# Kernel optimization log

Hardware: AMD Instinct MI355X
Metric: run time of the kernel (lower is better)

Reference implementation:

```python
import jax, jax.numpy as jnp
import numpy as np

N = 100000      # nodes
E = 1600000     # edges
D = 128         # embedding_size (num_heads=1)
L = 4           # num_layers
NEG_SLOPE_ATT = 0.2    # GATConv attention LeakyReLU
NEG_SLOPE_ACT = 0.01   # nn.LeakyReLU default
LN_EPS = 1e-5


def leaky(x, s):
    return jnp.where(x > 0, x, s * x)


def layer_norm(x, gamma, beta):
    mu = jnp.mean(x, axis=-1, keepdims=True)
    var = jnp.mean(jnp.square(x - mu), axis=-1, keepdims=True)
    return (x - mu) * jax.lax.rsqrt(var + LN_EPS) * gamma + beta


def gat_conv(x, src, dst, W, a_src, a_dst, b):
    # PyG GATConv, heads=1, add_self_loops=False, no edge features
    h = x @ W                                  # [N, D]
    alpha_src = h @ a_src                      # [N]
    alpha_dst = h @ a_dst                      # [N]
    e = leaky(alpha_src[src] + alpha_dst[dst], NEG_SLOPE_ATT)   # [E]
    # softmax over incoming edges of each destination node
    m = jax.ops.segment_max(e, dst, num_segments=N)             # [N]
    ex = jnp.exp(e - m[dst])
    denom = jax.ops.segment_sum(ex, dst, num_segments=N)        # [N]
    alpha = ex / (denom[dst] + 1e-16)                           # [E]
    out = jax.ops.segment_sum(alpha[:, None] * h[src], dst, num_segments=N)
    return out + b


def setup_inputs() -> dict:
    key = jax.random.key(0)
    ks = jax.random.split(key, 12)
    x = jax.random.normal(ks[0], (N, D), dtype=jnp.float32)
    edge_index = jax.random.randint(ks[1], (2, E), 0, N, dtype=jnp.int32)
    s = 0.05
    return {
        "x": x,
        "edge_index": edge_index,
        "W_in": jax.random.normal(ks[2], (D, D), dtype=jnp.float32) * s,
        "b_in": jnp.zeros((D,), dtype=jnp.float32),
        "Wl": jax.random.normal(ks[3], (L, D, D), dtype=jnp.float32) * s,
        "att_src": jax.random.normal(ks[4], (L, D), dtype=jnp.float32) * s,
        "att_dst": jax.random.normal(ks[5], (L, D), dtype=jnp.float32) * s,
        "bias_l": jnp.zeros((L, D), dtype=jnp.float32),
        "gamma": jnp.ones((L, D), dtype=jnp.float32),
        "beta": jnp.zeros((L, D), dtype=jnp.float32),
    }


def reference(x, edge_index, W_in, b_in, Wl, att_src, att_dst, bias_l, gamma, beta):
    src, dst = edge_index[0], edge_index[1]
    h = leaky(x @ W_in + b_in, NEG_SLOPE_ACT)
    for i in range(L):
        h = gat_conv(h, src, dst, Wl[i], att_src[i], att_dst[i], bias_l[i])
        h = layer_norm(h, gamma[i], beta[i])
        h = leaky(h, NEG_SLOPE_ACT)
        # dropout p=0.3 is identity in eval mode; pooling undefined in source -> identity
    return h
```

## Files before the change

### kernel.cpp

```cpp
#include <hip/hip_runtime.h>
#include <hip/hip_fp16.h>
#include <math.h>

#define NN 100000
#define EE 1600000
#define DD 128
#define NBUCK 196
#define NBLKP 196
#define EPB 8192

typedef _Float16 f16;
typedef f16 f16x8 __attribute__((ext_vector_type(8)));
typedef float f32x4 __attribute__((ext_vector_type(4)));

#define LDA 136
#define WCHUNKS 2304

__global__ __launch_bounds__(256) void part_hist_k(const int* __restrict__ dst, int* __restrict__ bcnt) {
    __shared__ int lc[NBUCK];
    int t = threadIdx.x, blk = blockIdx.x;
    if (t < NBUCK) lc[t] = 0;
    __syncthreads();
    int e0 = blk * EPB;
    for (int i = t; i < EPB; i += 256) {
        int e = e0 + i;
        if (e < EE) atomicAdd(&lc[dst[e] >> 9], 1);
    }
    __syncthreads();
    if (t < NBUCK) bcnt[t * NBLKP + blk] = lc[t];
}

__global__ __launch_bounds__(256) void scanBB_k(const int* __restrict__ bcnt, int* __restrict__ ebase,
                                                int* __restrict__ btot) {
    __shared__ int sh[256];
    int t = threadIdx.x, b = blockIdx.x;
    int c = (t < NBLKP) ? bcnt[b * NBLKP + t] : 0;
    sh[t] = c;
    __syncthreads();
    for (int off = 1; off < 256; off <<= 1) {
        int v = (t >= off) ? sh[t - off] : 0;
        __syncthreads();
        sh[t] += v;
        __syncthreads();
    }
    if (t < NBLKP) ebase[b * NBLKP + t] = sh[t] - c;
    if (t == 255) btot[b] = sh[255];
}

__global__ __launch_bounds__(256) void scanBT_k(const int* __restrict__ btot, int* __restrict__ bstart,
                                                int* __restrict__ offsets) {
    __shared__ int sh[256];
    int t = threadIdx.x;
    int c = (t < NBUCK) ? btot[t] : 0;
    sh[t] = c;
    __syncthreads();
    for (int off = 1; off < 256; off <<= 1) {
        int v = (t >= off) ? sh[t - off] : 0;
        __syncthreads();
        sh[t] += v;
        __syncthreads();
    }
    if (t < NBUCK) bstart[t] = sh[t] - c;
    if (t == 0) { bstart[NBUCK] = EE; offsets[NN] = EE; }
}

__global__ __launch_bounds__(256) void part_k(const int* __restrict__ src, const int* __restrict__ dst,
                                              const int* __restrict__ bstart, const int* __restrict__ ebase,
                                              int2* __restrict__ ebuf) {
    __shared__ int cur[NBUCK];
    int t = threadIdx.x, blk = blockIdx.x;
    if (t < NBUCK) cur[t] = bstart[t] + ebase[t * NBLKP + blk];
    __syncthreads();
    int e0 = blk * EPB;
    for (int i = t; i < EPB; i += 256) {
        int e = e0 + i;
        if (e < EE) {
            int s = src[e], d = dst[e];
            int p = atomicAdd(&cur[d >> 9], 1);
            ebuf[p] = make_int2(s, d);
        }
    }
}

__global__ __launch_bounds__(512) void bucket_sort_k(const int2* __restrict__ ebuf,
                                                     const int* __restrict__ bstart,
                                                     int* __restrict__ offsets,
                                                     int* __restrict__ ssrc,
                                                     int* __restrict__ sdst) {
    __shared__ int sh[512];
    __shared__ int cur[512];
    int t = threadIdx.x, b = blockIdx.x;
    int d0 = b << 9;
    int beg = bstart[b], end = bstart[b + 1];

    cur[t] = 0;
    __syncthreads();
    for (int e = beg + t; e < end; e += 512) atomicAdd(&cur[ebuf[e].y - d0], 1);
    __syncthreads();
    int c = cur[t];
    sh[t] = c;
    __syncthreads();
    for (int off = 1; off < 512; off <<= 1) {
        int v = (t >= off) ? sh[t - off] : 0;
        __syncthreads();
        sh[t] += v;
        __syncthreads();
    }
    int excl = sh[t] - c;
    if (d0 + t < NN) offsets[d0 + t] = beg + excl;
    cur[t] = beg + excl;
    __syncthreads();
    for (int e = beg + t; e < end; e += 512) {
        int2 ed = ebuf[e];
        int p = atomicAdd(&cur[ed.y - d0], 1);
        ssrc[p] = ed.x;
        sdst[p] = ed.y;
    }
}

__global__ __launch_bounds__(256) void wprep_k(const float* __restrict__ W_in,
                                               const float* __restrict__ Wl,
                                               f16* __restrict__ Wt) {
    int m = blockIdx.x;
    const float* src = (m == 0) ? W_in : (Wl + (size_t)(m - 1) * DD * DD);
    f16* dst = Wt + (size_t)m * (WCHUNKS * 8);
    for (int q = 0; q < 64; ++q) {
        int idx = q * 256 + threadIdx.x;
        int k = idx >> 7, n = idx & 127;
        dst[n * LDA + k] = (f16)src[idx];
    }
}

template <int MODE>
__global__ __launch_bounds__(256, 2) void gemm_k(const float* __restrict__ X,
                                                 const f16* __restrict__ Wt,
                                                 const float* __restrict__ bias,
                                                 const float* __restrict__ av_src,
                                                 const float* __restrict__ av_dst,
                                                 float* __restrict__ Yf,
                                                 __half* __restrict__ Yh,
                                                 float* __restrict__ alpha_src,
                                                 float* __restrict__ alpha_dst) {
    __shared__ __align__(16) f16 sAh[64 * LDA];
    __shared__ __align__(16) f16 sAl[64 * LDA];
    __shared__ __align__(16) f16 sWh[WCHUNKS * 8];
    int t = threadIdx.x;
    int w = t >> 6, lane = t & 63;
    int row0 = blockIdx.x * 64;

    {
        const uint4* wsrc = (const uint4*)Wt;
        uint4* wdst = (uint4*)sWh;
#pragma unroll
        for (int it = 0; it < 9; ++it) {
            int chunk = it * 256 + t;
            wdst[chunk] = wsrc[chunk];
        }
    }
#pragma unroll
    for (int q = 0; q < 4; ++q) {
        int id = q * 256 + t;
        int r = id >> 4, c = id & 15;
        int grow = row0 + r;
        float4 a = make_float4(0.f, 0.f, 0.f, 0.f), b = a;
        if (grow < NN) {
            const float4* p = (const float4*)(X + (size_t)grow * DD + c * 8);
            a = p[0]; b = p[1];
        }
        float xs[8] = {a.x, a.y, a.z, a.w, b.x, b.y, b.z, b.w};
        union { f16 h[8]; uint4 u; } H, L;
#pragma unroll
        for (int i = 0; i < 8; ++i) {
            f16 hv = (f16)xs[i];
            H.h[i] = hv;
            L.h[i] = (f16)(xs[i] - (float)hv);
        }
        int off = r * LDA + c * 8;
        *(uint4*)(sAh + off) = H.u;
        *(uint4*)(sAl + off) = L.u;
    }
    __syncthreads();

    int cl = lane & 15, qw = lane >> 4;
    f32x4 acc[8] = {};
    int aoff = (w * 16 + cl) * LDA;
#pragma unroll
    for (int ks = 0; ks < 4; ++ks) {
        int koff = ks * 32 + qw * 8;
        f16x8 ah = *(const f16x8*)(sAh + aoff + koff);
        f16x8 al = *(const f16x8*)(sAl + aoff + koff);
        f16x8 bh[8];
#pragma unroll
        for (int nf = 0; nf < 8; ++nf)
            bh[nf] = *(const f16x8*)(sWh + (nf * 16 + cl) * LDA + koff);
#pragma unroll
        for (int nf = 0; nf < 8; ++nf)
            acc[nf] = __builtin_amdgcn_mfma_f32_16x16x32_f16(ah, bh[nf], acc[nf], 0, 0, 0);
#pragma unroll
        for (int nf = 0; nf < 8; ++nf)
            acc[nf] = __builtin_amdgcn_mfma_f32_16x16x32_f16(al, bh[nf], acc[nf], 0, 0, 0);
    }

    int rbase = row0 + w * 16 + qw * 4;
    if (MODE == 0) {
        float bc[8];
#pragma unroll
        for (int nf = 0; nf < 8; ++nf) bc[nf] = bias[nf * 16 + cl];
#pragma unroll
        for (int i = 0; i < 4; ++i) {
            int row = rbase + i;
            if (row < NN) {
#pragma unroll
                for (int nf = 0; nf < 8; ++nf) {
                    float v = acc[nf][i] + bc[nf];
                    v = v > 0.f ? v : 0.01f * v;
                    Yf[(size_t)row * DD + nf * 16 + cl] = v;
                }
            }
        }
    } else {
        float as[8], ad[8];
#pragma unroll
        for (int nf = 0; nf < 8; ++nf) {
            as[nf] = av_src[nf * 16 + cl];
            ad[nf] = av_dst[nf * 16 + cl];
        }
        float pa[4] = {0.f, 0.f, 0.f, 0.f}, pb[4] = {0.f, 0.f, 0.f, 0.f};
#pragma unroll
        for (int nf = 0; nf < 8; ++nf) {
#pragma unroll
            for (int i = 0; i < 4; ++i) {
                float v = acc[nf][i];
                pa[i] += v * as[nf];
                pb[i] += v * ad[nf];
            }
        }
#pragma unroll
        for (int i = 0; i < 4; ++i) {
            int row = rbase + i;
            if (row < NN) {
#pragma unroll
                for (int nf = 0; nf < 8; ++nf)
                    Yh[(size_t)row * DD + nf * 16 + cl] = __float2half(acc[nf][i]);
            }
        }
#pragma unroll
        for (int i = 0; i < 4; ++i) {
#pragma unroll
            for (int off = 8; off >= 1; off >>= 1) {
                pa[i] += __shfl_xor(pa[i], off);
                pb[i] += __shfl_xor(pb[i], off);
            }
        }
        if (cl == 0) {
#pragma unroll
            for (int i = 0; i < 4; ++i) {
                int row = rbase + i;
                if (row < NN) {
                    alpha_src[row] = pa[i];
                    alpha_dst[row] = pb[i];
                }
            }
        }
    }
}

__global__ __launch_bounds__(256) void edgew_k(const int* __restrict__ ssrc,
                                               const int* __restrict__ sdst,
                                               const float* __restrict__ alpha_src,
                                               const float* __restrict__ alpha_dst,
                                               int2* __restrict__ epk) {
    int j = blockIdx.x * 256 + threadIdx.x;
    if (j < EE) {
        int s = ssrc[j];
        float e = alpha_src[s] + alpha_dst[sdst[j]];
        e = e > 0.f ? e : 0.2f * e;
        epk[j] = make_int2(s, __float_as_int(__expf(e)));
    }
}

__global__ __launch_bounds__(256) void agg_k(const __half* __restrict__ tmp,
                                             const int2* __restrict__ epk,
                                             const int* __restrict__ offsets,
                                             const float* __restrict__ bias,
                                             const float* __restrict__ gamma,
                                             const float* __restrict__ beta,
                                             float* __restrict__ out) {
    int wid = (blockIdx.x * 256 + threadIdx.x) >> 6;
    wid = __builtin_amdgcn_readfirstlane(wid);
    int lane = threadIdx.x & 63;
    int beg = __builtin_amdgcn_readfirstlane(offsets[wid]);
    int end = __builtin_amdgcn_readfirstlane(offsets[wid + 1]);

    const __half2* tmp2 = (const __half2*)tmp;
    float accAx = 0.f, accAy = 0.f, accBx = 0.f, accBy = 0.f;
    float dsum = 0.f;

    int j = beg;
    if (j < end && (j & 1)) {
        int2 p = epk[j];
        float w = __int_as_float(p.y);
        __half2 h = tmp2[(size_t)p.x * 64 + lane];
        dsum += w;
        accAx = fmaf(w, __half2float(h.x), accAx);
        accAy = fmaf(w, __half2float(h.y), accAy);
        ++j;
    }
    for (; j + 8 <= end; j += 8) {
        int4 q0 = *(const int4*)(epk + j);
        int4 q1 = *(const int4*)(epk + j + 2);
        int4 q2 = *(const int4*)(epk + j + 4);
        int4 q3 = *(const int4*)(epk + j + 6);
        __half2 h0 = tmp2[(size_t)q0.x * 64 + lane];
        __half2 h1 = tmp2[(size_t)q0.z * 64 + lane];
        __half2 h2 = tmp2[(size_t)q1.x * 64 + lane];
        __half2 h3 = tmp2[(size_t)q1.z * 64 + lane];
        __half2 h4 = tmp2[(size_t)q2.x * 64 + lane];
        __half2 h5 = tmp2[(size_t)q2.z * 64 + lane];
        __half2 h6 = tmp2[(size_t)q3.x * 64 + lane];
        __half2 h7 = tmp2[(size_t)q3.z * 64 + lane];
        float w0 = __int_as_float(q0.y), w1 = __int_as_float(q0.w);
        float w2 = __int_as_float(q1.y), w3 = __int_as_float(q1.w);
        float w4 = __int_as_float(q2.y), w5 = __int_as_float(q2.w);
        float w6 = __int_as_float(q3.y), w7 = __int_as_float(q3.w);
        dsum += ((w0 + w1) + (w2 + w3)) + ((w4 + w5) + (w6 + w7));
        accAx = fmaf(w0, __half2float(h0.x), accAx);
        accAy = fmaf(w0, __half2float(h0.y), accAy);
        accBx = fmaf(w1, __half2float(h1.x), accBx);
        accBy = fmaf(w1, __half2float(h1.y), accBy);
        accAx = fmaf(w2, __half2float(h2.x), accAx);
        accAy = fmaf(w2, __half2float(h2.y), accAy);
        accBx = fmaf(w3, __half2float(h3.x), accBx);
        accBy = fmaf(w3, __half2float(h3.y), accBy);
        accAx = fmaf(w4, __half2float(h4.x), accAx);
        accAy = fmaf(w4, __half2float(h4.y), accAy);
        accBx = fmaf(w5, __half2float(h5.x), accBx);
        accBy = fmaf(w5, __half2float(h5.y), accBy);
        accAx = fmaf(w6, __half2float(h6.x), accAx);
        accAy = fmaf(w6, __half2float(h6.y), accAy);
        accBx = fmaf(w7, __half2float(h7.x), accBx);
        accBy = fmaf(w7, __half2float(h7.y), accBy);
    }
    for (; j < end; ++j) {
        int2 p = epk[j];
        float w = __int_as_float(p.y);
        __half2 h = tmp2[(size_t)p.x * 64 + lane];
        dsum += w;
        accAx = fmaf(w, __half2float(h.x), accAx);
        accAy = fmaf(w, __half2float(h.y), accAy);
    }

    float inv = 1.0f / (dsum + 1e-16f);

    float ax = (accAx + accBx) * inv + bias[2 * lane];
    float ay = (accAy + accBy) * inv + bias[2 * lane + 1];

    float s1 = ax + ay;
#pragma unroll
    for (int off = 32; off >= 1; off >>= 1) s1 += __shfl_xor(s1, off);
    float mu = s1 * (1.0f / 128.0f);
    float dx = ax - mu, dy = ay - mu;
    float s2 = dx * dx + dy * dy;
#pragma unroll
    for (int off = 32; off >= 1; off >>= 1) s2 += __shfl_xor(s2, off);
    float rstd = rsqrtf(s2 * (1.0f / 128.0f) + 1e-5f);

    float yx = dx * rstd * gamma[2 * lane] + beta[2 * lane];
    float yy = dy * rstd * gamma[2 * lane + 1] + beta[2 * lane + 1];
    yx = yx > 0.f ? yx : 0.01f * yx;
    yy = yy > 0.f ? yy : 0.01f * yy;
    ((float2*)out)[(size_t)wid * 64 + lane] = make_float2(yx, yy);
}

extern "C" void kernel_launch(void* const* d_in, const int* in_sizes, int n_in,
                              void* d_out, int out_size, void* d_ws, size_t ws_size,
                              hipStream_t stream) {
    const float* x       = (const float*)d_in[0];
    const int*   ei      = (const int*)d_in[1];
    const float* W_in    = (const float*)d_in[2];
    const float* b_in    = (const float*)d_in[3];
    const float* Wl      = (const float*)d_in[4];
    const float* att_src = (const float*)d_in[5];
    const float* att_dst = (const float*)d_in[6];
    const float* bias_l  = (const float*)d_in[7];
    const float* gamma   = (const float*)d_in[8];
    const float* beta    = (const float*)d_in[9];
    float* out = (float*)d_out;

    char* ws = (char*)d_ws;
    __half* tmp      = (__half*)ws; ws += (size_t)NN * DD * 2;
    float* alpha_src = (float*)ws;  ws += (size_t)NN * 4;
    float* alpha_dst = (float*)ws;  ws += (size_t)NN * 4;
    int*   offsets   = (int*)ws;    ws += (size_t)(NN + 4) * 4;
    int*   ssrc      = (int*)ws;    ws += (size_t)EE * 4;
    int*   sdst      = (int*)ws;    ws += (size_t)EE * 4;
    int2*  ebuf      = (int2*)ws;   ws += (size_t)EE * 8;
    int*   bcnt      = (int*)ws;    ws += (size_t)NBUCK * NBLKP * 4;
    int*   ebase     = (int*)ws;    ws += (size_t)NBUCK * NBLKP * 4;
    int*   btot      = (int*)ws;    ws += (size_t)(NBUCK + 4) * 4;
    int*   bstart    = (int*)ws;    ws += (size_t)(NBUCK + 4) * 4;
    f16*   Wt        = (f16*)ws;    ws += (size_t)5 * WCHUNKS * 16;
    int2* epk = ebuf;

    const int* esrc = ei;
    const int* edst = ei + EE;

    part_hist_k<<<NBLKP, 256, 0, stream>>>(edst, bcnt);
    scanBB_k<<<NBUCK, 256, 0, stream>>>(bcnt, ebase, btot);
    scanBT_k<<<1, 256, 0, stream>>>(btot, bstart, offsets);
    part_k<<<NBLKP, 256, 0, stream>>>(esrc, edst, bstart, ebase, ebuf);
    bucket_sort_k<<<NBUCK, 512, 0, stream>>>(ebuf, bstart, offsets, ssrc, sdst);
    wprep_k<<<5, 256, 0, stream>>>(W_in, Wl, Wt);

    const int gg = (NN + 63) / 64;

    gemm_k<0><<<gg, 256, 0, stream>>>(x, Wt, b_in, nullptr, nullptr, out, nullptr, nullptr, nullptr);

    for (int i = 0; i < 4; i++) {
        gemm_k<1><<<gg, 256, 0, stream>>>(out, Wt + (size_t)(i + 1) * (WCHUNKS * 8), nullptr,
                                          att_src + (size_t)i * DD, att_dst + (size_t)i * DD,
                                          nullptr, tmp, alpha_src, alpha_dst);
        edgew_k<<<EE / 256, 256, 0, stream>>>(ssrc, sdst, alpha_src, alpha_dst, epk);
        agg_k<<<NN / 4, 256, 0, stream>>>(tmp, epk, offsets,
                                          bias_l + (size_t)i * DD, gamma + (size_t)i * DD,
                                          beta + (size_t)i * DD, out);
    }
}
```

Baseline: 605.6 us.

## Use fp16 intermediate activations, drop split-precision GEMM, widen GEMM tiles

Intermediate layer activations are now kept in fp16 in the output buffer rather than fp32. The GEMM reads them directly and no longer does the hi/lo split that doubled the MFMA count. Each GEMM block now covers 128 rows with two row fragments per wave, and the aggregation loop is rewritten as a single 16-edge unrolled loop with masking plus padded edge entries. This cuts activation traffic and MFMA work at the cost of some fp16 accuracy in the hidden states.

```diff
diff --git a/kernel.cpp b/kernel.cpp
--- a/kernel.cpp
+++ b/kernel.cpp
@@ -131,90 +131,93 @@
     }
 }
 
-template <int MODE>
-__global__ __launch_bounds__(256, 2) void gemm_k(const float* __restrict__ X,
+template <int MODE, int F32IN>
+__global__ __launch_bounds__(256, 2) void gemm_k(const void* __restrict__ Xv,
                                                  const f16* __restrict__ Wt,
                                                  const float* __restrict__ bias,
                                                  const float* __restrict__ av_src,
                                                  const float* __restrict__ av_dst,
-                                                 float* __restrict__ Yf,
                                                  __half* __restrict__ Yh,
                                                  float* __restrict__ alpha_src,
                                                  float* __restrict__ alpha_dst) {
-    __shared__ __align__(16) f16 sAh[64 * LDA];
-    __shared__ __align__(16) f16 sAl[64 * LDA];
-    __shared__ __align__(16) f16 sWh[WCHUNKS * 8];
+    __shared__ __align__(16) f16 sA[128 * LDA];
+    __shared__ __align__(16) f16 sW[WCHUNKS * 8];
     int t = threadIdx.x;
     int w = t >> 6, lane = t & 63;
-    int row0 = blockIdx.x * 64;
+    int row0 = blockIdx.x * 128;
 
     {
         const uint4* wsrc = (const uint4*)Wt;
-        uint4* wdst = (uint4*)sWh;
-#pragma unroll
-        for (int it = 0; it < 9; ++it) {
-            int chunk = it * 256 + t;
-            wdst[chunk] = wsrc[chunk];
-        }
-    }
-#pragma unroll
-    for (int q = 0; q < 4; ++q) {
-        int id = q * 256 + t;
-        int r = id >> 4, c = id & 15;
-        int grow = row0 + r;
-        float4 a = make_float4(0.f, 0.f, 0.f, 0.f), b = a;
-        if (grow < NN) {
-            const float4* p = (const float4*)(X + (size_t)grow * DD + c * 8);
-            a = p[0]; b = p[1];
-        }
-        float xs[8] = {a.x, a.y, a.z, a.w, b.x, b.y, b.z, b.w};
-        union { f16 h[8]; uint4 u; } H, L;
-#pragma unroll
-        for (int i = 0; i < 8; ++i) {
-            f16 hv = (f16)xs[i];
-            H.h[i] = hv;
-            L.h[i] = (f16)(xs[i] - (float)hv);
-        }
-        int off = r * LDA + c * 8;
-        *(uint4*)(sAh + off) = H.u;
-        *(uint4*)(sAl + off) = L.u;
+        uint4* wdst = (uint4*)sW;
+#pragma unroll
+        for (int it = 0; it < 9; ++it) wdst[it * 256 + t] = wsrc[it * 256 + t];
+    }
+    if (F32IN) {
+        const float* X = (const float*)Xv;
+#pragma unroll
+        for (int q = 0; q < 8; ++q) {
+            int id = q * 256 + t;
+            int r = id >> 4, c = id & 15;
+            int grow = row0 + r;
+            float4 a = make_float4(0.f, 0.f, 0.f, 0.f), b = a;
+            if (grow < NN) {
+                const float4* p = (const float4*)(X + (size_t)grow * DD + c * 8);
+                a = p[0]; b = p[1];
+            }
+            union { f16 h[8]; uint4 u; } H;
+            H.h[0] = (f16)a.x; H.h[1] = (f16)a.y; H.h[2] = (f16)a.z; H.h[3] = (f16)a.w;
+            H.h[4] = (f16)b.x; H.h[5] = (f16)b.y; H.h[6] = (f16)b.z; H.h[7] = (f16)b.w;
+            *(uint4*)(sA + r * LDA + c * 8) = H.u;
+        }
+    } else {
+        const __half* X = (const __half*)Xv;
+#pragma unroll
+        for (int q = 0; q < 8; ++q) {
+            int id = q * 256 + t;
+            int r = id >> 4, c = id & 15;
+            int grow = row0 + r;
+            uint4 v = make_uint4(0, 0, 0, 0);
+            if (grow < NN) v = ((const uint4*)(X + (size_t)grow * DD))[c];
+            *(uint4*)(sA + r * LDA + c * 8) = v;
+        }
     }
     __syncthreads();
 
     int cl = lane & 15, qw = lane >> 4;
-    f32x4 acc[8] = {};
-    int aoff = (w * 16 + cl) * LDA;
+    f32x4 acc[2][8] = {};
 #pragma unroll
     for (int ks = 0; ks < 4; ++ks) {
         int koff = ks * 32 + qw * 8;
-        f16x8 ah = *(const f16x8*)(sAh + aoff + koff);
-        f16x8 al = *(const f16x8*)(sAl + aoff + koff);
         f16x8 bh[8];
 #pragma unroll
         for (int nf = 0; nf < 8; ++nf)
-            bh[nf] = *(const f16x8*)(sWh + (nf * 16 + cl) * LDA + koff);
-#pragma unroll
-        for (int nf = 0; nf < 8; ++nf)
-            acc[nf] = __builtin_amdgcn_mfma_f32_16x16x32_f16(ah, bh[nf], acc[nf], 0, 0, 0);
-#pragma unroll
-        for (int nf = 0; nf < 8; ++nf)
-            acc[nf] = __builtin_amdgcn_mfma_f32_16x16x32_f16(al, bh[nf], acc[nf], 0, 0, 0);
-    }
-
-    int rbase = row0 + w * 16 + qw * 4;
+            bh[nf] = *(const f16x8*)(sW + (nf * 16 + cl) * LDA + koff);
+#pragma unroll
+        for (int rf = 0; rf < 2; ++rf) {
+            f16x8 ah = *(const f16x8*)(sA + (w * 32 + rf * 16 + cl) * LDA + koff);
+#pragma unroll
+            for (int nf = 0; nf < 8; ++nf)
+                acc[rf][nf] = __builtin_amdgcn_mfma_f32_16x16x32_f16(ah, bh[nf], acc[rf][nf], 0, 0, 0);
+        }
+    }
+
     if (MODE == 0) {
         float bc[8];
 #pragma unroll
         for (int nf = 0; nf < 8; ++nf) bc[nf] = bias[nf * 16 + cl];
 #pragma unroll
-        for (int i = 0; i < 4; ++i) {
-            int row = rbase + i;
-            if (row < NN) {
-#pragma unroll
-                for (int nf = 0; nf < 8; ++nf) {
-                    float v = acc[nf][i] + bc[nf];
-                    v = v > 0.f ? v : 0.01f * v;
-                    Yf[(size_t)row * DD + nf * 16 + cl] = v;
+        for (int rf = 0; rf < 2; ++rf) {
+            int rbase = row0 + w * 32 + rf * 16 + qw * 4;
+#pragma unroll
+            for (int i = 0; i < 4; ++i) {
+                int row = rbase + i;
+                if (row < NN) {
+#pragma unroll
+                    for (int nf = 0; nf < 8; ++nf) {
+                        float v = acc[rf][nf][i] + bc[nf];
+                        v = v > 0.f ? v : 0.01f * v;
+                        Yh[(size_t)row * DD + nf * 16 + cl] = __float2half(v);
+                    }
                 }
             }
         }
@@ -225,40 +228,44 @@
             as[nf] = av_src[nf * 16 + cl];
             ad[nf] = av_dst[nf * 16 + cl];
         }
-        float pa[4] = {0.f, 0.f, 0.f, 0.f}, pb[4] = {0.f, 0.f, 0.f, 0.f};
-#pragma unroll
-        for (int nf = 0; nf < 8; ++nf) {
-#pragma unroll
-            for (int i = 0; i < 4; ++i) {
-                float v = acc[nf][i];
-                pa[i] += v * as[nf];
-                pb[i] += v * ad[nf];
-            }
-        }
-#pragma unroll
-        for (int i = 0; i < 4; ++i) {
-            int row = rbase + i;
-            if (row < NN) {
-#pragma unroll
-                for (int nf = 0; nf < 8; ++nf)
-                    Yh[(size_t)row * DD + nf * 16 + cl] = __float2half(acc[nf][i]);
-            }
-        }
-#pragma unroll
-        for (int i = 0; i < 4; ++i) {
-#pragma unroll
-            for (int off = 8; off >= 1; off >>= 1) {
-                pa[i] += __shfl_xor(pa[i], off);
-                pb[i] += __shfl_xor(pb[i], off);
-            }
-        }
-        if (cl == 0) {
+#pragma unroll
+        for (int rf = 0; rf < 2; ++rf) {
+            int rbase = row0 + w * 32 + rf * 16 + qw * 4;
+            float pa[4] = {0.f, 0.f, 0.f, 0.f}, pb[4] = {0.f, 0.f, 0.f, 0.f};
+#pragma unroll
+            for (int nf = 0; nf < 8; ++nf) {
+#pragma unroll
+                for (int i = 0; i < 4; ++i) {
+                    float v = acc[rf][nf][i];
+                    pa[i] += v * as[nf];
+                    pb[i] += v * ad[nf];
+                }
+            }
 #pragma unroll
             for (int i = 0; i < 4; ++i) {
                 int row = rbase + i;
                 if (row < NN) {
-                    alpha_src[row] = pa[i];
-                    alpha_dst[row] = pb[i];
+#pragma unroll
+                    for (int nf = 0; nf < 8; ++nf)
+                        Yh[(size_t)row * DD + nf * 16 + cl] = __float2half(acc[rf][nf][i]);
+                }
+            }
+#pragma unroll
+            for (int i = 0; i < 4; ++i) {
+#pragma unroll
+                for (int off = 8; off >= 1; off >>= 1) {
+                    pa[i] += __shfl_xor(pa[i], off);
+                    pb[i] += __shfl_xor(pb[i], off);
+                }
+            }
+            if (cl == 0) {
+#pragma unroll
+                for (int i = 0; i < 4; ++i) {
+                    int row = rbase + i;
+                    if (row < NN) {
+                        alpha_src[row] = pa[i];
+                        alpha_dst[row] = pb[i];
+                    }
                 }
             }
         }
@@ -276,16 +283,19 @@
         float e = alpha_src[s] + alpha_dst[sdst[j]];
         e = e > 0.f ? e : 0.2f * e;
         epk[j] = make_int2(s, __float_as_int(__expf(e)));
-    }
-}
-
+    } else if (j < EE + 16) {
+        epk[j] = make_int2(0, 0);
+    }
+}
+
+template <int HOUT>
 __global__ __launch_bounds__(256) void agg_k(const __half* __restrict__ tmp,
                                              const int2* __restrict__ epk,
                                              const int* __restrict__ offsets,
                                              const float* __restrict__ bias,
                                              const float* __restrict__ gamma,
                                              const float* __restrict__ beta,
-                                             float* __restrict__ out) {
+                                             void* __restrict__ outv) {
     int wid = (blockIdx.x * 256 + threadIdx.x) >> 6;
     wid = __builtin_amdgcn_readfirstlane(wid);
     int lane = threadIdx.x & 63;
@@ -293,67 +303,37 @@
     int end = __builtin_amdgcn_readfirstlane(offsets[wid + 1]);
 
     const __half2* tmp2 = (const __half2*)tmp;
-    float accAx = 0.f, accAy = 0.f, accBx = 0.f, accBy = 0.f;
-    float dsum = 0.f;
-
-    int j = beg;
-    if (j < end && (j & 1)) {
-        int2 p = epk[j];
-        float w = __int_as_float(p.y);
-        __half2 h = tmp2[(size_t)p.x * 64 + lane];
-        dsum += w;
-        accAx = fmaf(w, __half2float(h.x), accAx);
-        accAy = fmaf(w, __half2float(h.y), accAy);
-        ++j;
-    }
-    for (; j + 8 <= end; j += 8) {
-        int4 q0 = *(const int4*)(epk + j);
-        int4 q1 = *(const int4*)(epk + j + 2);
-        int4 q2 = *(const int4*)(epk + j + 4);
-        int4 q3 = *(const int4*)(epk + j + 6);
-        __half2 h0 = tmp2[(size_t)q0.x * 64 + lane];
-        __half2 h1 = tmp2[(size_t)q0.z * 64 + lane];
-        __half2 h2 = tmp2[(size_t)q1.x * 64 + lane];
-        __half2 h3 = tmp2[(size_t)q1.z * 64 + lane];
-        __half2 h4 = tmp2[(size_t)q2.x * 64 + lane];
-        __half2 h5 = tmp2[(size_t)q2.z * 64 + lane];
-        __half2 h6 = tmp2[(size_t)q3.x * 64 + lane];
-        __half2 h7 = tmp2[(size_t)q3.z * 64 + lane];
-        float w0 = __int_as_float(q0.y), w1 = __int_as_float(q0.w);
-        float w2 = __int_as_float(q1.y), w3 = __int_as_float(q1.w);
-        float w4 = __int_as_float(q2.y), w5 = __int_as_float(q2.w);
-        float w6 = __int_as_float(q3.y), w7 = __int_as_float(q3.w);
-        dsum += ((w0 + w1) + (w2 + w3)) + ((w4 + w5) + (w6 + w7));
-        accAx = fmaf(w0, __half2float(h0.x), accAx);
-        accAy = fmaf(w0, __half2float(h0.y), accAy);
-        accBx = fmaf(w1, __half2float(h1.x), accBx);
-        accBy = fmaf(w1, __half2float(h1.y), accBy);
-        accAx = fmaf(w2, __half2float(h2.x), accAx);
-        accAy = fmaf(w2, __half2float(h2.y), accAy);
-        accBx = fmaf(w3, __half2float(h3.x), accBx);
-        accBy = fmaf(w3, __half2float(h3.y), accBy);
-        accAx = fmaf(w4, __half2float(h4.x), accAx);
-        accAy = fmaf(w4, __half2float(h4.y), accAy);
-        accBx = fmaf(w5, __half2float(h5.x), accBx);
-        accBy = fmaf(w5, __half2float(h5.y), accBy);
-        accAx = fmaf(w6, __half2float(h6.x), accAx);
-        accAy = fmaf(w6, __half2float(h6.y), accAy);
-        accBx = fmaf(w7, __half2float(h7.x), accBx);
-        accBy = fmaf(w7, __half2float(h7.y), accBy);
-    }
-    for (; j < end; ++j) {
-        int2 p = epk[j];
-        float w = __int_as_float(p.y);
-        __half2 h = tmp2[(size_t)p.x * 64 + lane];
-        dsum += w;
-        accAx = fmaf(w, __half2float(h.x), accAx);
-        accAy = fmaf(w, __half2float(h.y), accAy);
+    float ax0 = 0.f, ay0 = 0.f, ax1 = 0.f, ay1 = 0.f, dsum = 0.f;
+
+    for (int j = (beg & ~1); j < end; j += 16) {
+        int4 q[8];
+#pragma unroll
+        for (int k = 0; k < 8; ++k) q[k] = *(const int4*)(epk + j + 2 * k);
+        __half2 h[16];
+#pragma unroll
+        for (int k = 0; k < 8; ++k) {
+            h[2 * k]     = tmp2[(size_t)q[k].x * 64 + lane];
+            h[2 * k + 1] = tmp2[(size_t)q[k].z * 64 + lane];
+        }
+#pragma unroll
+        for (int k = 0; k < 8; ++k) {
+            int e0 = j + 2 * k, e1 = e0 + 1;
+            bool v0 = (k == 0) ? (e0 >= beg && e0 < end) : (e0 < end);
+            bool v1 = (e1 < end);
+            float w0 = v0 ? __int_as_float(q[k].y) : 0.f;
+            float w1 = v1 ? __int_as_float(q[k].w) : 0.f;
+            dsum += w0 + w1;
+            ax0 = fmaf(w0, __half2float(h[2 * k].x), ax0);
+            ay0 = fmaf(w0, __half2float(h[2 * k].y), ay0);
+            ax1 = fmaf(w1, __half2float(h[2 * k + 1].x), ax1);
+            ay1 = fmaf(w1, __half2float(h[2 * k + 1].y), ay1);
+        }
     }
 
     float inv = 1.0f / (dsum + 1e-16f);
 
-    float ax = (accAx + accBx) * inv + bias[2 * lane];
-    float ay = (accAy + accBy) * inv + bias[2 * lane + 1];
+    float ax = (ax0 + ax1) * inv + bias[2 * lane];
+    float ay = (ay0 + ay1) * inv + bias[2 * lane + 1];
 
     float s1 = ax + ay;
 #pragma unroll
@@ -369,7 +349,11 @@
     float yy = dy * rstd * gamma[2 * lane + 1] + beta[2 * lane + 1];
     yx = yx > 0.f ? yx : 0.01f * yx;
     yy = yy > 0.f ? yy : 0.01f * yy;
-    ((float2*)out)[(size_t)wid * 64 + lane] = make_float2(yx, yy);
+    if (HOUT) {
+        ((__half2*)outv)[(size_t)wid * 64 + lane] = __floats2half2_rn(yx, yy);
+    } else {
+        ((float2*)outv)[(size_t)wid * 64 + lane] = make_float2(yx, yy);
+    }
 }
 
 extern "C" void kernel_launch(void* const* d_in, const int* in_sizes, int n_in,
@@ -394,7 +378,7 @@
     int*   offsets   = (int*)ws;    ws += (size_t)(NN + 4) * 4;
     int*   ssrc      = (int*)ws;    ws += (size_t)EE * 4;
     int*   sdst      = (int*)ws;    ws += (size_t)EE * 4;
-    int2*  ebuf      = (int2*)ws;   ws += (size_t)EE * 8;
+    int2*  ebuf      = (int2*)ws;   ws += (size_t)(EE + 16) * 8;
     int*   bcnt      = (int*)ws;    ws += (size_t)NBUCK * NBLKP * 4;
     int*   ebase     = (int*)ws;    ws += (size_t)NBUCK * NBLKP * 4;
     int*   btot      = (int*)ws;    ws += (size_t)(NBUCK + 4) * 4;
@@ -402,6 +386,8 @@
     f16*   Wt        = (f16*)ws;    ws += (size_t)5 * WCHUNKS * 16;
     int2* epk = ebuf;
 
+    __half* hbuf = (__half*)d_out;
+
     const int* esrc = ei;
     const int* edst = ei + EE;
 
@@ -412,17 +398,24 @@
     bucket_sort_k<<<NBUCK, 512, 0, stream>>>(ebuf, bstart, offsets, ssrc, sdst);
     wprep_k<<<5, 256, 0, stream>>>(W_in, Wl, Wt);
 
-    const int gg = (NN + 63) / 64;
-
-    gemm_k<0><<<gg, 256, 0, stream>>>(x, Wt, b_in, nullptr, nullptr, out, nullptr, nullptr, nullptr);
+    const int gg = (NN + 127) / 128;
+    const int eg = (EE + 16 + 255) / 256;
+
+    gemm_k<0, 1><<<gg, 256, 0, stream>>>(x, Wt, b_in, nullptr, nullptr, hbuf, nullptr, nullptr);
 
     for (int i = 0; i < 4; i++) {
-        gemm_k<1><<<gg, 256, 0, stream>>>(out, Wt + (size_t)(i + 1) * (WCHUNKS * 8), nullptr,
-                                          att_src + (size_t)i * DD, att_dst + (size_t)i * DD,
-                                          nullptr, tmp, alpha_src, alpha_dst);
-        edgew_k<<<EE / 256, 256, 0, stream>>>(ssrc, sdst, alpha_src, alpha_dst, epk);
-        agg_k<<<NN / 4, 256, 0, stream>>>(tmp, epk, offsets,
-                                          bias_l + (size_t)i * DD, gamma + (size_t)i * DD,
-                                          beta + (size_t)i * DD, out);
-    }
-}
+        gemm_k<1, 0><<<gg, 256, 0, stream>>>(hbuf, Wt + (size_t)(i + 1) * (WCHUNKS * 8), nullptr,
+                                             att_src + (size_t)i * DD, att_dst + (size_t)i * DD,
+                                             tmp, alpha_src, alpha_dst);
+        edgew_k<<<eg, 256, 0, stream>>>(ssrc, sdst, alpha_src, alpha_dst, epk);
+        if (i < 3) {
+            agg_k<1><<<NN / 4, 256, 0, stream>>>(tmp, epk, offsets,
+                                                 bias_l + (size_t)i * DD, gamma + (size_t)i * DD,
+                                                 beta + (size_t)i * DD, (void*)hbuf);
+        } else {
+            agg_k<0><<<NN / 4, 256, 0, stream>>>(tmp, epk, offsets,
+                                                 bias_l + (size_t)i * DD, gamma + (size_t)i * DD,
+                                                 beta + (size_t)i * DD, (void*)out);
+        }
+    }
+}
```

Result: faster. 580.4 us (-4.2%).
